# Performance work log

Hardware: AMD Instinct MI355X
Metric: run time of the kernel (lower is better)

## Reference

```python
import jax, jax.numpy as jnp
import numpy as np
from jax import lax

NUM_CLASSES = 80
STRIDES = (8, 16, 32, 64, 128)
PRE_NMS_THRESH = 0.05
PRE_NMS_TOPK = 1000
NMS_THRESH = 0.6
POST_NMS_TOPK = 100
NUM_CONVS = 4
CIN = 256
BATCH = 2
FEAT_SHAPES = ((100, 152), (50, 76), (25, 38), (13, 19), (7, 10))
CLASS_OFFSET = 10000.0  # coordinate offset for class-aware NMS


def conv3x3(x, w, b):
    # x: [B,C,H,W], w: [O,C,3,3] -> [B,O,H,W], stride 1, SAME padding
    y = lax.conv_general_dilated(x, w, (1, 1), 'SAME',
                                 dimension_numbers=('NCHW', 'OIHW', 'NCHW'))
    return y + b[None, :, None, None]


def tower(x, Ws, Bs):
    # sequence of (conv3x3 -> ReLU), norm='none'
    for i in range(Ws.shape[0]):
        x = jax.nn.relu(conv3x3(x, Ws[i], Bs[i]))
    return x


def compute_locations(h, w, stride):
    sx = jnp.arange(w, dtype=jnp.float32) * stride
    sy = jnp.arange(h, dtype=jnp.float32) * stride
    yy, xx = jnp.meshgrid(sy, sx, indexing='ij')
    return jnp.stack([xx.reshape(-1), yy.reshape(-1)], axis=1) + stride // 2  # [HW,2]


def nms_single(boxes, scores, classes):
    # boxes [N,4], scores [N] (>=0), classes [N] int. Greedy class-aware NMS.
    off = classes.astype(boxes.dtype) * CLASS_OFFSET
    b = boxes + off[:, None]
    area = (b[:, 2] - b[:, 0]) * (b[:, 3] - b[:, 1])

    def step(s, _):
        i = jnp.argmax(s)
        v = s[i]
        bi = b[i]
        lt = jnp.maximum(bi[:2], b[:, :2])
        rb = jnp.minimum(bi[2:], b[:, 2:])
        wh = jnp.maximum(rb - lt, 0.0)
        inter = wh[:, 0] * wh[:, 1]
        iou = inter / (area[i] + area - inter + 1e-9)
        s2 = jnp.where(iou > NMS_THRESH, -1.0, s).at[i].set(-1.0)
        return s2, (i, v)

    _, (idx, vals) = lax.scan(step, scores, None, length=POST_NMS_TOPK)
    valid = vals > 0.0
    out = jnp.concatenate(
        [boxes[idx], vals[:, None], classes[idx].astype(boxes.dtype)[:, None]], axis=1)
    return jnp.where(valid[:, None], out, 0.0)  # [POST_NMS_TOPK, 6]


def _forward(p3, p4, p5, p6, p7, cls_w, cls_b, box_w, box_b,
             logit_w, logit_b, pred_w, pred_b, ctr_w, ctr_b, scales):
    feats = (p3, p4, p5, p6, p7)
    boxes_all, scores_all, cls_all = [], [], []
    for l, x in enumerate(feats):
        # share_tower has 0 convs -> identity
        ct = tower(x, cls_w, cls_b)
        bt = tower(x, box_w, box_b)
        logits = conv3x3(ct, logit_w, logit_b)                   # [B,C,H,W]
        ctr = conv3x3(bt, ctr_w, ctr_b)                          # [B,1,H,W]
        reg = jax.nn.relu(conv3x3(bt, pred_w, pred_b) * scales[l])  # [B,4,H,W]
        B, _, H, W = logits.shape
        HW = H * W
        locs = compute_locations(H, W, STRIDES[l])               # [HW,2]
        cls_prob = jax.nn.sigmoid(logits).transpose(0, 2, 3, 1).reshape(B, HW, NUM_CLASSES)
        ctr_prob = jax.nn.sigmoid(ctr).reshape(B, HW, 1)
        s = cls_prob * ctr_prob                                  # thresh_with_ctr
        s = jnp.where(s > PRE_NMS_THRESH, s, 0.0)
        k = min(PRE_NMS_TOPK, HW * NUM_CLASSES)
        vals, idx = lax.top_k(s.reshape(B, HW * NUM_CLASSES), k)
        loc_idx = idx // NUM_CLASSES                             # [B,k]
        cls_idx = idx % NUM_CLASSES
        reg_f = reg.transpose(0, 2, 3, 1).reshape(B, HW, 4)
        reg_sel = jnp.take_along_axis(reg_f, loc_idx[..., None], axis=1)  # [B,k,4]
        loc_sel = locs[loc_idx]                                  # [B,k,2]
        boxes = jnp.stack([loc_sel[..., 0] - reg_sel[..., 0],
                           loc_sel[..., 1] - reg_sel[..., 1],
                           loc_sel[..., 0] + reg_sel[..., 2],
                           loc_sel[..., 1] + reg_sel[..., 3]], axis=-1)
        boxes_all.append(boxes)
        scores_all.append(jnp.sqrt(jnp.maximum(vals, 1e-12)))
        cls_all.append(cls_idx)
    boxes = jnp.concatenate(boxes_all, axis=1)    # [B,N,4]
    scores = jnp.concatenate(scores_all, axis=1)  # [B,N]
    classes = jnp.concatenate(cls_all, axis=1)    # [B,N]
    return jax.vmap(nms_single)(boxes, scores, classes)  # [B,POST_NMS_TOPK,6]


def setup_inputs() -> dict:
    key = jax.random.key(0)
    ks = jax.random.split(key, 12)
    std = 0.05  # larger than fcos init std=0.01 so decoded scores exceed the threshold
    inp = {}
    for i, (h, w) in enumerate(FEAT_SHAPES):
        inp[f'p{i + 3}'] = jax.random.normal(ks[i], (BATCH, CIN, h, w), dtype=jnp.float32)
    inp['cls_w'] = jax.random.normal(ks[5], (NUM_CONVS, CIN, CIN, 3, 3), dtype=jnp.float32) * std
    inp['cls_b'] = jnp.zeros((NUM_CONVS, CIN), dtype=jnp.float32)
    inp['box_w'] = jax.random.normal(ks[6], (NUM_CONVS, CIN, CIN, 3, 3), dtype=jnp.float32) * std
    inp['box_b'] = jnp.zeros((NUM_CONVS, CIN), dtype=jnp.float32)
    inp['logit_w'] = jax.random.normal(ks[7], (NUM_CLASSES, CIN, 3, 3), dtype=jnp.float32) * std
    inp['logit_b'] = jnp.zeros((NUM_CLASSES,), dtype=jnp.float32)
    inp['pred_w'] = jax.random.normal(ks[8], (4, CIN, 3, 3), dtype=jnp.float32) * std
    inp['pred_b'] = jnp.zeros((4,), dtype=jnp.float32)
    inp['ctr_w'] = jax.random.normal(ks[9], (1, CIN, 3, 3), dtype=jnp.float32) * std
    inp['ctr_b'] = jnp.zeros((1,), dtype=jnp.float32)
    inp['scales'] = jnp.ones((5,), dtype=jnp.float32)
    return inp


def reference(p3, p4, p5, p6, p7, cls_w, cls_b, box_w, box_b,
              logit_w, logit_b, pred_w, pred_b, ctr_w, ctr_b, scales):
    return _forward(p3, p4, p5, p6, p7, cls_w, cls_b, box_w, box_b,
                    logit_w, logit_b, pred_w, pred_b, ctr_w, ctr_b, scales)
```

## Files before the change

kernel.cpp:

```cpp
#include <hip/hip_runtime.h>
#include <stdint.h>
#include <math.h>

#define NCLS 80
#define TOTHW 20267

typedef _Float16 f16x8 __attribute__((ext_vector_type(8)));
typedef float f32x4 __attribute__((ext_vector_type(4)));
typedef short s16x8 __attribute__((ext_vector_type(8)));

static constexpr int cLW[5]    = {152,76,38,19,10};
static constexpr int cLH[5]    = {100,50,25,13,7};
static constexpr int cLHW[5]   = {15200,3800,950,247,70};
static constexpr int cLCUM[5]  = {0,15200,19000,19950,20197};
static constexpr int cLSTR[5]  = {8,16,32,64,128};
static constexpr int cCB[11]   = {0,123,246,278,310,319,328,331,334,335,336};
static constexpr int cPBASE[11]= {0,15744,31488,35584,39680,40832,41984,42368,42752,42880,43008};
static constexpr int cRCUM[11] = {0,100,200,250,300,325,350,363,376,383,390};
static constexpr int cCPX64[6] = {0,475,594,624,632,635};
#define NPXB64 635
#define SBE 11010048ull

__device__ __forceinline__ void split2(float y, unsigned short& h0, unsigned short& h1) {
  _Float16 b0 = (_Float16)y;
  float f0 = (float)b0;
  _Float16 b1 = (_Float16)((y - f0) * 2048.0f);
  h0 = __builtin_bit_cast(unsigned short, b0);
  h1 = __builtin_bit_cast(unsigned short, b1);
}

__device__ __forceinline__ void lds_hist_add(uint32_t* h, uint32_t bucket) {
  unsigned long long act = __ballot(1);
  int lane = (int)(threadIdx.x & 63u);
  int leader = __ffsll(act) - 1;
  uint32_t lb = (uint32_t)__shfl((int)bucket, leader, 64);
  unsigned long long same = __ballot(bucket == lb);
  if (same == act) {
    if (lane == leader) atomicAdd(&h[bucket], (uint32_t)__popcll(act));
  } else {
    atomicAdd(&h[bucket], 1u);
  }
}

__global__ void k_zero(unsigned short* X0, unsigned short* X1) {
  int px = blockIdx.x * 256 + threadIdx.x;
  if (px >= 43008) return;
  int pi = 0;
#pragma unroll
  for (int i = 1; i < 10; i++) if (px >= cPBASE[i]) pi = i;
  const int l = pi >> 1;
  const int p = px - cPBASE[pi];
  const int W = cLW[l], H = cLH[l], PWl = W + 2;
  const int pr = p / PWl, pc = p - pr * PWl;
  if (pr >= 1 && pr <= H && pc >= 1 && pc <= W) return;
  s16x8 z = {0,0,0,0,0,0,0,0};
  size_t base = (size_t)px * 256;
#pragma unroll
  for (int k = 0; k < 32; k++) {
    *reinterpret_cast<s16x8*>(X0 + base + k*8) = z;
    *reinterpret_cast<s16x8*>(X1 + base + k*8) = z;
  }
}

__global__ __launch_bounds__(256)
void k_prep(const float* __restrict__ p0, const float* __restrict__ p1,
            const float* __restrict__ p2, const float* __restrict__ p3,
            const float* __restrict__ p4,
            unsigned short* __restrict__ X0, unsigned short* __restrict__ X1) {
  int bx = blockIdx.x;
  int pi = 0;
#pragma unroll
  for (int i = 1; i < 10; i++) if (bx >= cRCUM[i]) pi = i;
  const int h = bx - cRCUM[pi];
  const int l = pi >> 1, bidx = pi & 1;
  const int W = cLW[l], HW = cLHW[l], PWl = W + 2;
  const int PB = cPBASE[pi];
  const float* src;
  if (l == 0) src = p0; else if (l == 1) src = p1; else if (l == 2) src = p2;
  else if (l == 3) src = p3; else src = p4;
  src += (size_t)bidx * 256 * HW;
  const int tid = threadIdx.x;
  __shared__ float tile[64][152];
  for (int c0 = 0; c0 < 256; c0 += 64) {
    {
      int c = tid >> 2, wq = tid & 3;
      for (int w = wq; w < W; w += 4)
        tile[c][w] = src[(size_t)(c0 + c) * HW + h * W + w];
    }
    __syncthreads();
    {
      int c8 = (tid & 7) * 8;
      for (int w = tid >> 3; w < W; w += 32) {
        size_t base = (size_t)(PB + (h + 1) * PWl + (w + 1)) * 256 + c0 + c8;
        unsigned short a0[8], a1[8];
#pragma unroll
        for (int j = 0; j < 8; j++) split2(tile[c8 + j][w], a0[j], a1[j]);
        *reinterpret_cast<s16x8*>(X0 + base) = *reinterpret_cast<s16x8*>(a0);
        *reinterpret_cast<s16x8*>(X1 + base) = *reinterpret_cast<s16x8*>(a1);
      }
    }
    __syncthreads();
  }
}

__global__ void k_pack(const float* __restrict__ w, unsigned short* __restrict__ wp) {
  const int oc = blockIdx.x, c = threadIdx.x;
#pragma unroll
  for (int r = 0; r < 9; r++) {
    float v = w[((size_t)oc * 256 + c) * 9 + r];
    unsigned short h0, h1;
    split2(v, h0, h1);
    wp[((size_t)(r * 2 + 0) * 256 + oc) * 256 + c] = h0;
    wp[((size_t)(r * 2 + 1) * 256 + oc) * 256 + c] = h1;
  }
}

__global__ void k_packhead(const float* __restrict__ ctw, const float* __restrict__ pdw,
                           float* __restrict__ wh) {
  const int r = blockIdx.x, c = threadIdx.x;
  float* d = &wh[((size_t)r * 256 + c) * 5];
  d[0] = ctw[c * 9 + r];
#pragma unroll
  for (int q = 0; q < 4; q++) d[1 + q] = pdw[(size_t)q * 2304 + c * 9 + r];
}

struct MfArgs {
  const unsigned short *X0, *X1;
  const unsigned short *Wp;
  const float* bias;
  unsigned short *Y0, *Y1;
  float* actf;
  float* scores;
  const float* ctrp;
  uint32_t* hist;
};

template<int EPI>
__global__ __launch_bounds__(256, 2)
void conv_mfma(MfArgs a) {
  __shared__ __align__(16) unsigned short lds[18432];
  const int tid = threadIdx.x;
  const int lane = tid & 63;
  const int wid = tid >> 6;

  const int nwg = (EPI == 2) ? 336 : 672;
  const int id = blockIdx.x;
  const int w = (id & 7) * (nwg >> 3) + (id >> 3);
  const int oc0 = (EPI == 2) ? 0 : (w & 1) * 128;
  int bx = (EPI == 2) ? w : (w >> 1);

  int pi = 0;
#pragma unroll
  for (int i = 1; i < 10; i++) if (bx >= cCB[i]) pi = i;
  const int l = pi >> 1, bidx = pi & 1;
  const int pxb = bx - cCB[pi];
  const int px0 = pxb * 128;
  const int PB = cPBASE[pi];
  const int W = cLW[l], H = cLH[l], HW = cLHW[l], PWl = W + 2;

  int row_[2], g_[2];
#pragma unroll
  for (int d = 0; d < 2; d++) {
    int idx2 = tid + d * 256;
    row_[d] = idx2 >> 2;
    g_[d] = idx2 & 3;
  }

  const int wr = wid >> 1, wc = wid & 1;
  const int kg = lane >> 4, ln15 = lane & 15;
  int fA[4], fB[4];
#pragma unroll
  for (int mt = 0; mt < 4; mt++) fA[mt] = (wr * 64 + mt * 16 + ln15) * 72 + kg * 8;
#pragma unroll
  for (int nt = 0; nt < 4; nt++) fB[nt] = 9216 + (wc * 64 + nt * 16 + ln15) * 72 + kg * 8;

  f32x4 acc0[4][4], acc1[4][4];
#pragma unroll
  for (int mt = 0; mt < 4; mt++)
#pragma unroll
    for (int nt = 0; nt < 4; nt++) {
      acc0[mt][nt] = (f32x4){0.f, 0.f, 0.f, 0.f};
      acc1[mt][nt] = (f32x4){0.f, 0.f, 0.f, 0.f};
    }

  s16x8 ra[4], rb[4];
  auto loadstep = [&](int step) {
    const int rr = step >> 3;
    const int c0 = (step & 7) << 5;
    const int dh = rr / 3 - 1, dw = rr - (rr / 3) * 3 - 1;
    const long long OFF = (long long)(PB + px0 + dh * PWl + dw);
#pragma unroll
    for (int s = 0; s < 2; s++) {
      const unsigned short* Xs = (s == 0) ? a.X0 : a.X1;
      const unsigned short* Ws = a.Wp + (size_t)(rr * 2 + s) * 65536;
#pragma unroll
      for (int d = 0; d < 2; d++) {
        ra[s * 2 + d] = *reinterpret_cast<const s16x8*>(Xs + (OFF + row_[d]) * 256 + c0 + g_[d] * 8);
        rb[s * 2 + d] = *reinterpret_cast<const s16x8*>(Ws + (size_t)(oc0 + row_[d]) * 256 + c0 + g_[d] * 8);
      }
    }
  };

  loadstep(0);
  for (int step = 0; step < 72; ++step) {
    if (step) __syncthreads();
#pragma unroll
    for (int s = 0; s < 2; s++)
#pragma unroll
      for (int d = 0; d < 2; d++) {
        const int o = row_[d] * 72 + (s * 4 + g_[d]) * 8;
        *reinterpret_cast<s16x8*>(&lds[o]) = ra[s * 2 + d];
        *reinterpret_cast<s16x8*>(&lds[o + 9216]) = rb[s * 2 + d];
      }
    __syncthreads();
    if (step != 71) loadstep(step + 1);

    f16x8 bv[4][2];
#pragma unroll
    for (int nt = 0; nt < 4; nt++) {
      bv[nt][0] = *reinterpret_cast<const f16x8*>(&lds[fB[nt]]);
      bv[nt][1] = *reinterpret_cast<const f16x8*>(&lds[fB[nt] + 32]);
    }
#pragma unroll
    for (int mt = 0; mt < 4; mt++) {
      f16x8 av0 = *reinterpret_cast<const f16x8*>(&lds[fA[mt]]);
      f16x8 av1 = *reinterpret_cast<const f16x8*>(&lds[fA[mt] + 32]);
#pragma unroll
      for (int nt = 0; nt < 4; nt++) {
        acc0[mt][nt] = __builtin_amdgcn_mfma_f32_16x16x32_f16(av0, bv[nt][0], acc0[mt][nt], 0, 0, 0);
        acc1[mt][nt] = __builtin_amdgcn_mfma_f32_16x16x32_f16(av0, bv[nt][1], acc1[mt][nt], 0, 0, 0);
        acc1[mt][nt] = __builtin_amdgcn_mfma_f32_16x16x32_f16(av1, bv[nt][0], acc1[mt][nt], 0, 0, 0);
      }
    }
  }
  __syncthreads();

  uint32_t* hh = nullptr;
  if (EPI == 2) {
    hh = reinterpret_cast<uint32_t*>(lds);
    for (int i = tid; i < 4096; i += 256) hh[i] = 0;
    __syncthreads();
  }
#pragma unroll
  for (int mt = 0; mt < 4; mt++) {
#pragma unroll
    for (int i = 0; i < 4; i++) {
      const int pxl = wr * 64 + mt * 16 + (lane >> 4) * 4 + i;
      const int p = px0 + pxl;
      const int pr = p / PWl, pc = p - pr * PWl;
      if (!(pr >= 1 && pr <= H && pc >= 1 && pc <= W)) continue;
      const int hw = (pr - 1) * W + (pc - 1);
#pragma unroll
      for (int nt = 0; nt < 4; nt++) {
        const int oc = oc0 + wc * 64 + nt * 16 + ln15;
        const float v = acc0[mt][nt][i] + acc1[mt][nt][i] * 4.8828125e-4f;
        if (EPI == 2) {
          if (oc < NCLS) {
            float y = v + a.bias[oc];
            float pcs = 1.0f / (1.0f + expf(-y));
            float s = pcs * a.ctrp[2 * cLCUM[l] + bidx * HW + hw];
            s = (s > 0.05f) ? s : 0.f;
            a.scores[(size_t)NCLS * (2 * cLCUM[l] + bidx * HW) + (size_t)oc * HW + hw] = s;
            lds_hist_add(hh, __float_as_uint(s) >> 20);
          }
        } else {
          float y = fmaxf(v + a.bias[oc], 0.f);
          if (EPI == 0) {
            size_t o = (size_t)(PB + p) * 256 + oc;
            unsigned short h0, h1;
            split2(y, h0, h1);
            a.Y0[o] = h0; a.Y1[o] = h1;
          } else {
            a.actf[(size_t)(PB + p) * 256 + oc] = y;
          }
        }
      }
    }
  }
  if (EPI == 2) {
    __syncthreads();
    uint32_t* gh = a.hist + (size_t)(l * 2 + bidx) * 4096;
    for (int i = tid; i < 4096; i += 256) { uint32_t v = hh[i]; if (v) atomicAdd(&gh[i], v); }
  }
}

__global__ __launch_bounds__(256)
void k_head2(const float* __restrict__ headact, const float* __restrict__ wh,
             const float* __restrict__ ctb, const float* __restrict__ pdb,
             const float* __restrict__ scl,
             float* __restrict__ ctrp, float* __restrict__ regb) {
  __shared__ float swh[11520];
  for (int i = threadIdx.x; i < 11520; i += 256) swh[i] = wh[i];
  int bx = blockIdx.x; int l = 0;
#pragma unroll
  for (int i = 1; i < 5; i++) if (bx >= cCPX64[i]) l = i;
  const int lblk = bx - cCPX64[l];
  const int H = cLH[l], W = cLW[l], HW = cLHW[l]; const int N = 2 * HW;
  const int lane = threadIdx.x & 63;
  const int wv = threadIdx.x >> 6;
  __syncthreads();
  const float bb0 = ctb[0], bb1 = pdb[0], bb2 = pdb[1], bb3 = pdb[2], bb4 = pdb[3];
  const float sc = scl[l];
  const int c4 = lane * 4;
  for (int t = 0; t < 16; ++t) {
    int px = lblk * 64 + wv * 16 + t;
    if (px >= N) break;
    int bb = px / HW; int hw = px - bb * HW; int hh = hw / W; int ww = hw - hh * W;
    const int PB = cPBASE[l * 2 + bb];
    float a0 = 0.f, a1 = 0.f, a2 = 0.f, a3 = 0.f, a4 = 0.f;
#pragma unroll
    for (int r = 0; r < 9; r++) {
      int dh = r / 3 - 1, dw = r % 3 - 1;
      int ih = hh + dh, iw = ww + dw;
      if (!(((unsigned)ih < (unsigned)H) && ((unsigned)iw < (unsigned)W))) continue;
      const float4 x = *reinterpret_cast<const float4*>(
          headact + (size_t)(PB + (ih + 1) * (W + 2) + (iw + 1)) * 256 + c4);
      const float* wr = &swh[(size_t)(r * 256 + c4) * 5];
      a0 = fmaf(x.x, wr[0],  a0); a1 = fmaf(x.x, wr[1],  a1); a2 = fmaf(x.x, wr[2],  a2);
      a3 = fmaf(x.x, wr[3],  a3); a4 = fmaf(x.x, wr[4],  a4);
      a0 = fmaf(x.y, wr[5],  a0); a1 = fmaf(x.y, wr[6],  a1); a2 = fmaf(x.y, wr[7],  a2);
      a3 = fmaf(x.y, wr[8],  a3); a4 = fmaf(x.y, wr[9],  a4);
      a0 = fmaf(x.z, wr[10], a0); a1 = fmaf(x.z, wr[11], a1); a2 = fmaf(x.z, wr[12], a2);
      a3 = fmaf(x.z, wr[13], a3); a4 = fmaf(x.z, wr[14], a4);
      a0 = fmaf(x.w, wr[15], a0); a1 = fmaf(x.w, wr[16], a1); a2 = fmaf(x.w, wr[17], a2);
      a3 = fmaf(x.w, wr[18], a3); a4 = fmaf(x.w, wr[19], a4);
    }
#pragma unroll
    for (int off = 32; off > 0; off >>= 1) {
      a0 += __shfl_xor(a0, off, 64); a1 += __shfl_xor(a1, off, 64); a2 += __shfl_xor(a2, off, 64);
      a3 += __shfl_xor(a3, off, 64); a4 += __shfl_xor(a4, off, 64);
    }
    if (lane == 0) {
      const int gi = 2 * cLCUM[l] + bb * HW + hw;
      ctrp[gi] = 1.0f / (1.0f + expf(-(a0 + bb0)));
      float* rg = regb + (size_t)gi * 4;
      rg[0] = fmaxf((a1 + bb1) * sc, 0.f);
      rg[1] = fmaxf((a2 + bb2) * sc, 0.f);
      rg[2] = fmaxf((a3 + bb3) * sc, 0.f);
      rg[3] = fmaxf((a4 + bb4) * sc, 0.f);
    }
  }
}

__global__ void k_init(uint32_t* __restrict__ hist, uint32_t* __restrict__ ctrA,
                       uint32_t* __restrict__ ctrB) {
  int i = blockIdx.x * blockDim.x + threadIdx.x;
  if (i < 40960) hist[i] = 0;
  if (i < 10) { ctrA[i] = 0; ctrB[i] = 0; }
}

__global__ __launch_bounds__(256)
void k_select(const uint32_t* __restrict__ hist, int* __restrict__ meta) {
  const int sid = blockIdx.x;
  const uint32_t* gh = hist + (size_t)sid * 4096;
  __shared__ uint32_t ps[256];
  uint32_t sum = 0;
  for (int i = 0; i < 16; i++) sum += gh[threadIdx.x * 16 + i];
  ps[threadIdx.x] = sum;
  __syncthreads();
  if (threadIdx.x == 0) {
    uint32_t c = 0; int T = 0, m = 1000;
    for (int ch = 255; ch >= 0; --ch) {
      if (c + ps[ch] >= 1000u) {
        for (int t = ch * 16 + 15; t >= ch * 16; --t) {
          uint32_t hv = gh[t];
          if (c + hv >= 1000u) { T = t; m = (int)(1000u - c); break; }
          c += hv;
        }
        break;
      }
      c += ps[ch];
    }
    meta[sid * 4 + 0] = T;
    meta[sid * 4 + 1] = (int)c;
    meta[sid * 4 + 2] = m;
    meta[sid * 4 + 3] = (int)gh[T];
  }
}

__global__ __launch_bounds__(256)
void k_collect(const float* __restrict__ scores, const int* __restrict__ meta,
               unsigned long long* __restrict__ listA, unsigned long long* __restrict__ listB,
               uint32_t* __restrict__ ctrA, uint32_t* __restrict__ ctrB) {
  const int sid = blockIdx.y; const int l = sid >> 1, b = sid & 1;
  const int HW = cLHW[l]; const int size = NCLS * HW;
  const int base = blockIdx.x * 4096;
  if (base >= size) return;
  const size_t sbase = (size_t)NCLS * (2 * cLCUM[l] + b * HW);
  const float* sb = scores + sbase;
  unsigned long long* lB = listB + sbase;
  unsigned long long* lA = listA + (size_t)sid * 1024;
  const uint32_t T = (uint32_t)meta[sid * 4];
  const int lane = (int)(threadIdx.x & 63u);
  __shared__ uint32_t cA, cB, bA, bB;
  if (threadIdx.x == 0) { cA = 0; cB = 0; }
  __syncthreads();
  uint32_t wa = 0, wb = 0;
  for (int j = 0; j < 16; j++) {
    int i = base + threadIdx.x + j * 256;
    bool inb = (i < size);
    uint32_t bits = inb ? __float_as_uint(sb[i]) : 0u;
    uint32_t bkt = bits >> 20;
    unsigned long long mA = __ballot(inb && bkt > T);
    unsigned long long mB = __ballot(inb && bkt == T);
    if (lane == 0) { wa += (uint32_t)__popcll(mA); wb += (uint32_t)__popcll(mB); }
  }
  if (lane == 0) { if (wa) atomicAdd(&cA, wa); if (wb) atomicAdd(&cB, wb); }
  __syncthreads();
  if (threadIdx.x == 0) {
    bA = cA ? atomicAdd(&ctrA[sid], cA) : 0u;
    bB = cB ? atomicAdd(&ctrB[sid], cB) : 0u;
    cA = 0; cB = 0;
  }
  __syncthreads();
  for (int j = 0; j < 16; j++) {
    int i = base + threadIdx.x + j * 256;
    bool inb = (i < size);
    uint32_t bits = inb ? __float_as_uint(sb[i]) : 0u;
    uint32_t bkt = bits >> 20;
    bool pA = inb && bkt > T;
    bool pB = inb && bkt == T;
    unsigned long long key = 0;
    if (pA || pB) {
      int cls = i / HW; int hw = i - cls * HW;
      uint32_t idx = (uint32_t)(hw * NCLS + cls);
      key = ((unsigned long long)bits << 32) | (unsigned long long)(0xFFFFFFFFu - idx);
    }
    unsigned long long mA = __ballot(pA);
    unsigned long long mB = __ballot(pB);
    unsigned long long lt = (1ull << lane) - 1ull;
    if (mA) {
// ... 32 lines not shown
  unsigned long long prefix = 0, mask = 0;
  for (int p = 7; p >= 0; --p) {
    for (int i = threadIdx.x; i < 256; i += 1024) h[i] = 0;
    __syncthreads();
    for (int i = threadIdx.x; i < nB; i += 1024) {
      unsigned long long k = lB[i];
      if ((k & mask) == prefix) {
        uint32_t bkt = (uint32_t)((k >> (p * 8)) & 255ull);
        lds_hist_add(h, bkt);
      }
    }
    __syncthreads();
    if (threadIdx.x == 0) {
      uint32_t c = 0; int sel = 0; int mnew = m;
      for (int t = 255; t >= 0; --t) {
        if (c + h[t] >= (uint32_t)m) { sel = t; mnew = m - (int)c; break; }
        c += h[t];
      }
      sPre = prefix | ((unsigned long long)sel << (p * 8));
      sM = mnew;
    }
    __syncthreads();
    prefix = sPre; m = sM;
    mask |= (0xFFull << (p * 8));
    __syncthreads();
  }
  if (threadIdx.x == 0) sCnt = ctrA[sid];
  __syncthreads();
  for (int i = threadIdx.x; i < nB; i += 1024) {
    unsigned long long k = lB[i];
    if (k >= prefix) {
      uint32_t pos = atomicAdd(&sCnt, 1u);
      if (pos < 1024u) listA[(size_t)sid * 1024 + pos] = k;
    }
  }
  __syncthreads();
  if (threadIdx.x == 0) ctrA[sid] = sCnt;
}

__global__ __launch_bounds__(256)
void k_sortdec(const unsigned long long* __restrict__ listA, const uint32_t* __restrict__ ctrA,
               const float* __restrict__ regb, float* __restrict__ cbox,
               float* __restrict__ cscr, float* __restrict__ ccls) {
  const int sid = blockIdx.x; const int l = sid >> 1, b = sid & 1;
  const int HW = cLHW[l], W = cLW[l];
  __shared__ unsigned long long key[1024];
  int n = (int)ctrA[sid]; if (n > 1024) n = 1024;
  for (int i = threadIdx.x; i < 1024; i += 256)
    key[i] = (i < n) ? listA[(size_t)sid * 1024 + i] : 0ull;
  __syncthreads();
  for (int len = 2; len <= 1024; len <<= 1) {
    for (int j = len >> 1; j > 0; j >>= 1) {
      for (int t = threadIdx.x; t < 512; t += 256) {
        int i = ((t & ~(j - 1)) << 1) | (t & (j - 1));
        int pp = i | j;
        unsigned long long a = key[i], bq = key[pp];
        bool desc = ((i & len) == 0);
        if ((a < bq) == desc) { key[i] = bq; key[pp] = a; }
      }
      __syncthreads();
    }
  }
  for (int r = threadIdx.x; r < 1000; r += 256) {
    unsigned long long k = key[r];
    uint32_t bits = (uint32_t)(k >> 32);
    uint32_t idx = 0xFFFFFFFFu - (uint32_t)(k & 0xFFFFFFFFull);
    float val = __uint_as_float(bits);
    float sc = sqrtf(fmaxf(val, 1e-12f));
    int cls = (int)(idx % NCLS); int loc = (int)(idx / NCLS);
    int hh = loc / W; int ww = loc - hh * W;
    float cx = (float)(ww * cLSTR[l] + (cLSTR[l] >> 1));
    float cy = (float)(hh * cLSTR[l] + (cLSTR[l] >> 1));
    const float* rg = regb + (size_t)(2 * cLCUM[l] + b * HW + loc) * 4;
    int slot = b * 5000 + l * 1000 + r;
    cbox[slot * 4 + 0] = cx - rg[0];
    cbox[slot * 4 + 1] = cy - rg[1];
    cbox[slot * 4 + 2] = cx + rg[2];
    cbox[slot * 4 + 3] = cy + rg[3];
    cscr[slot] = sc;
    ccls[slot] = (float)cls;
  }
}

__global__ __launch_bounds__(1024)
void k_nms(const float* __restrict__ cbox, const float* __restrict__ cscr,
           const float* __restrict__ ccls, float* __restrict__ out) {
  const int b = blockIdx.x;
  const int tid = threadIdx.x;
  __shared__ float s[5000];
  __shared__ float wv[16]; __shared__ int wi[16];
  __shared__ float bbx[5]; __shared__ int sBi; __shared__ float sBv;
  float x1[5], y1[5], x2[5], y2[5], ar[5];
#pragma unroll
  for (int r = 0; r < 5; r++) {
    int j = tid + r * 1024;
    if (j < 5000) {
      const float4 bx = *reinterpret_cast<const float4*>(cbox + ((size_t)b * 5000 + j) * 4);
      float off = ccls[b * 5000 + j] * 10000.0f;
      x1[r] = bx.x + off; y1[r] = bx.y + off; x2[r] = bx.z + off; y2[r] = bx.w + off;
      ar[r] = (x2[r] - x1[r]) * (y2[r] - y1[r]);
      s[j] = cscr[b * 5000 + j];
    }
  }
  __syncthreads();
  for (int it = 0; it < 100; ++it) {
    float best = -1e30f; int bi = 0x7FFFFFFF;
#pragma unroll
    for (int r = 0; r < 5; r++) {
      int j = tid + r * 1024;
      if (j < 5000) {
        float v = s[j];
        if (v > best || (v == best && j < bi)) { best = v; bi = j; }
      }
    }
    for (int o = 32; o > 0; o >>= 1) {
      float ov = __shfl_down(best, o, 64); int oi = __shfl_down(bi, o, 64);
      if (ov > best || (ov == best && oi < bi)) { best = ov; bi = oi; }
    }
    if ((tid & 63) == 0) { wv[tid >> 6] = best; wi[tid >> 6] = bi; }
    __syncthreads();
    if (tid < 64) {
      float v = (tid < 16) ? wv[tid] : -1e30f; int ix = (tid < 16) ? wi[tid] : 0x7FFFFFFF;
      for (int o = 8; o > 0; o >>= 1) {
        float ov = __shfl_down(v, o, 64); int oi = __shfl_down(ix, o, 64);
        if (ov > v || (ov == v && oi < ix)) { v = ov; ix = oi; }
      }
      if (tid == 0) { sBi = ix; sBv = v; }
    }
    __syncthreads();
    const int pick = sBi; const float pv = sBv;
    if (tid == (pick & 1023)) {
      const int r = pick >> 10;
      bbx[0] = x1[r]; bbx[1] = y1[r]; bbx[2] = x2[r]; bbx[3] = y2[r]; bbx[4] = ar[r];
      float* orow = out + ((size_t)b * 100 + it) * 6;
      if (pv > 0.f) {
        const float4 obx = *reinterpret_cast<const float4*>(cbox + ((size_t)b * 5000 + pick) * 4);
        orow[0] = obx.x; orow[1] = obx.y; orow[2] = obx.z; orow[3] = obx.w;
        orow[4] = pv; orow[5] = ccls[b * 5000 + pick];
      } else {
        orow[0] = 0.f; orow[1] = 0.f; orow[2] = 0.f; orow[3] = 0.f; orow[4] = 0.f; orow[5] = 0.f;
      }
    }
    __syncthreads();
    const float bx1 = bbx[0], by1 = bbx[1], bx2 = bbx[2], by2 = bbx[3], ba = bbx[4];
#pragma unroll
    for (int r = 0; r < 5; r++) {
      int j = tid + r * 1024;
      if (j < 5000) {
        float ix1 = fmaxf(bx1, x1[r]), iy1 = fmaxf(by1, y1[r]);
        float ix2 = fminf(bx2, x2[r]), iy2 = fminf(by2, y2[r]);
        float iw = fmaxf(ix2 - ix1, 0.f), ih = fmaxf(iy2 - iy1, 0.f);
        float inter = iw * ih;
        float iou = inter / ((ba + ar[r] - inter) + 1e-9f);
        if (iou > 0.6f || j == pick) s[j] = -1.0f;
      }
    }
    __syncthreads();
  }
}

static inline size_t alignup(size_t x) { return (x + 255) & ~(size_t)255; }

extern "C" void kernel_launch(void* const* d_in, const int* in_sizes, int n_in,
                              void* d_out, int out_size, void* d_ws, size_t ws_size,
                              hipStream_t stream) {
  (void)in_sizes; (void)n_in; (void)out_size; (void)ws_size;
  const float* p0 = (const float*)d_in[0];
  const float* p1 = (const float*)d_in[1];
  const float* p2 = (const float*)d_in[2];
  const float* p3 = (const float*)d_in[3];
  const float* p4 = (const float*)d_in[4];
  const float* cls_w   = (const float*)d_in[5];
  const float* cls_b   = (const float*)d_in[6];
  const float* box_w   = (const float*)d_in[7];
  const float* box_b   = (const float*)d_in[8];
  const float* logit_w = (const float*)d_in[9];
  const float* logit_b = (const float*)d_in[10];
  const float* pred_w  = (const float*)d_in[11];
  const float* pred_b  = (const float*)d_in[12];
  const float* ctr_w   = (const float*)d_in[13];
  const float* ctr_b   = (const float*)d_in[14];
  const float* scales  = (const float*)d_in[15];

  char* base = (char*)d_ws;
  size_t off = 0;
  auto take = [&](size_t bytes) { void* p = base + off; off = alignup(off + bytes); return p; };
  float* regb = (float*)take((size_t)4 * 2 * TOTHW * 4);
  float* ctrp = (float*)take((size_t)2 * TOTHW * 4);
  uint32_t* hist = (uint32_t*)take((size_t)40960 * 4);
  int* meta = (int*)take((size_t)40 * 4);
  uint32_t* ctrA = (uint32_t*)take(256);
  uint32_t* ctrB = (uint32_t*)take(256);
  unsigned long long* listA = (unsigned long long*)take((size_t)10 * 1024 * 8);
  float* cbox = (float*)take((size_t)2 * 5000 * 16);
  float* cscr = (float*)take((size_t)2 * 5000 * 4);
  float* ccls = (float*)take((size_t)2 * 5000 * 4);
  float* wh   = (float*)take((size_t)9 * 256 * 5 * 4);
  unsigned short* wpack = (unsigned short*)take((size_t)9 * 2 * 256 * 256 * 2);
  unsigned short* R1_0 = (unsigned short*)take(SBE * 2);
  unsigned short* R1_1 = (unsigned short*)take(SBE * 2);
  unsigned short* R2_0 = (unsigned short*)take(SBE * 2);
  unsigned short* R2_1 = (unsigned short*)take(SBE * 2);
  (void)take(65536);
  float* scores = (float*)R2_0;
  unsigned long long* listB = (unsigned long long*)R1_0;
  float* headact = (float*)R1_0;

  const size_t WSTRIDE = (size_t)256 * 2304;

  hipLaunchKernelGGL(k_init, dim3(160), dim3(256), 0, stream, hist, ctrA, ctrB);
  hipLaunchKernelGGL(k_packhead, dim3(9), dim3(256), 0, stream, ctr_w, pred_w, wh);
  hipLaunchKernelGGL(k_zero, dim3(168), dim3(256), 0, stream, R1_0, R1_1);
  hipLaunchKernelGGL(k_zero, dim3(168), dim3(256), 0, stream, R2_0, R2_1);
  hipLaunchKernelGGL(k_prep, dim3(390), dim3(256), 0, stream, p0, p1, p2, p3, p4, R1_0, R1_1);

  auto runConv = [&](int epi, const unsigned short* x0, const unsigned short* x1,
                     const float* bias, unsigned short* y0, unsigned short* y1,
                     float* af, float* sc) {
    MfArgs a;
    a.X0 = x0; a.X1 = x1; a.Wp = wpack; a.bias = bias;
    a.Y0 = y0; a.Y1 = y1; a.actf = af; a.scores = sc; a.ctrp = ctrp;
    a.hist = hist;
    if (epi == 0)      hipLaunchKernelGGL(conv_mfma<0>, dim3(672), dim3(256), 0, stream, a);
    else if (epi == 1) hipLaunchKernelGGL(conv_mfma<1>, dim3(672), dim3(256), 0, stream, a);
    else               hipLaunchKernelGGL(conv_mfma<2>, dim3(336), dim3(256), 0, stream, a);
  };

  hipLaunchKernelGGL(k_pack, dim3(256), dim3(256), 0, stream, box_w + 0 * WSTRIDE, wpack);
  runConv(0, R1_0, R1_1, box_b + 0,   R2_0, R2_1, nullptr, nullptr);
  hipLaunchKernelGGL(k_pack, dim3(256), dim3(256), 0, stream, box_w + 1 * WSTRIDE, wpack);
  runConv(0, R2_0, R2_1, box_b + 256, R1_0, R1_1, nullptr, nullptr);
  hipLaunchKernelGGL(k_pack, dim3(256), dim3(256), 0, stream, box_w + 2 * WSTRIDE, wpack);
  runConv(0, R1_0, R1_1, box_b + 512, R2_0, R2_1, nullptr, nullptr);
  hipLaunchKernelGGL(k_pack, dim3(256), dim3(256), 0, stream, box_w + 3 * WSTRIDE, wpack);
  runConv(1, R2_0, R2_1, box_b + 768, nullptr, nullptr, headact, nullptr);
  hipLaunchKernelGGL(k_head2, dim3(NPXB64), dim3(256), 0, stream, headact, wh, ctr_b,
                     pred_b, scales, ctrp, regb);

  hipLaunchKernelGGL(k_zero, dim3(168), dim3(256), 0, stream, R1_0, R1_1);
  hipLaunchKernelGGL(k_prep, dim3(390), dim3(256), 0, stream, p0, p1, p2, p3, p4, R1_0, R1_1);
  hipLaunchKernelGGL(k_pack, dim3(256), dim3(256), 0, stream, cls_w + 0 * WSTRIDE, wpack);
  runConv(0, R1_0, R1_1, cls_b + 0,   R2_0, R2_1, nullptr, nullptr);
  hipLaunchKernelGGL(k_pack, dim3(256), dim3(256), 0, stream, cls_w + 1 * WSTRIDE, wpack);
  runConv(0, R2_0, R2_1, cls_b + 256, R1_0, R1_1, nullptr, nullptr);
  hipLaunchKernelGGL(k_pack, dim3(256), dim3(256), 0, stream, cls_w + 2 * WSTRIDE, wpack);
  runConv(0, R1_0, R1_1, cls_b + 512, R2_0, R2_1, nullptr, nullptr);
  hipLaunchKernelGGL(k_pack, dim3(256), dim3(256), 0, stream, cls_w + 3 * WSTRIDE, wpack);
  runConv(0, R2_0, R2_1, cls_b + 768, R1_0, R1_1, nullptr, nullptr);
  hipLaunchKernelGGL(k_pack, dim3(80), dim3(256), 0, stream, logit_w, wpack);
  runConv(2, R1_0, R1_1, logit_b, nullptr, nullptr, nullptr, scores);

  hipLaunchKernelGGL(k_select,  dim3(10), dim3(256), 0, stream, hist, meta);
  hipLaunchKernelGGL(k_collect, dim3(297, 10), dim3(256), 0, stream, scores, meta, listA, listB, ctrA, ctrB);
  hipLaunchKernelGGL(k_refine,  dim3(10), dim3(1024), 0, stream, meta, listB, listA, ctrA);
  hipLaunchKernelGGL(k_sortdec, dim3(10), dim3(256), 0, stream, listA, ctrA, regb, cbox, cscr, ccls);
  hipLaunchKernelGGL(k_nms,     dim3(2), dim3(1024), 0, stream, cbox, cscr, ccls, (float*)d_out);
}
```

Baseline: 2.245 ms.

## Channel-block activation layout, direct-to-register MFMA loads, prepacked weights, per-class parallel NMS

Activations move to a channel-chunked layout (8 chunks of 32 channels) and weights are pre-swizzled into MFMA fragment order, so the conv kernel loads operands straight from global memory into registers. This drops the LDS staging and the per-step barriers. All nine weight layers are packed once in a single launch instead of before each conv. The serial 100-iteration greedy NMS is replaced by a per-class parallel NMS followed by a radix top-100 selection, which is exact because offset boxes of different classes never overlap. The risk is that losing LDS reuse raises global and L2 traffic, since each wave now refetches its A and B fragments.

```diff
diff --git a/kernel.cpp b/kernel.cpp
--- a/kernel.cpp
+++ b/kernel.cpp
@@ -4,6 +4,8 @@
 
 #define NCLS 80
 #define TOTHW 20267
+#define CHS 1376256
+#define WLAYER 1179648ull
 
 typedef _Float16 f16x8 __attribute__((ext_vector_type(8)));
 typedef float f32x4 __attribute__((ext_vector_type(4)));
@@ -54,11 +56,14 @@
   const int pr = p / PWl, pc = p - pr * PWl;
   if (pr >= 1 && pr <= H && pc >= 1 && pc <= W) return;
   s16x8 z = {0,0,0,0,0,0,0,0};
-  size_t base = (size_t)px * 256;
-#pragma unroll
-  for (int k = 0; k < 32; k++) {
-    *reinterpret_cast<s16x8*>(X0 + base + k*8) = z;
-    *reinterpret_cast<s16x8*>(X1 + base + k*8) = z;
+#pragma unroll
+  for (int ch = 0; ch < 8; ch++) {
+    size_t base = (size_t)ch * CHS + (size_t)px * 32;
+#pragma unroll
+    for (int q = 0; q < 4; q++) {
+      *reinterpret_cast<s16x8*>(X0 + base + q*8) = z;
+      *reinterpret_cast<s16x8*>(X1 + base + q*8) = z;
+    }
   }
 }
 
@@ -90,8 +95,10 @@
     __syncthreads();
     {
       int c8 = (tid & 7) * 8;
+      const int c = c0 + c8;
+      const size_t cb = (size_t)(c >> 5) * CHS + (c & 31);
       for (int w = tid >> 3; w < W; w += 32) {
-        size_t base = (size_t)(PB + (h + 1) * PWl + (w + 1)) * 256 + c0 + c8;
+        size_t base = cb + (size_t)(PB + (h + 1) * PWl + (w + 1)) * 32;
         unsigned short a0[8], a1[8];
 #pragma unroll
         for (int j = 0; j < 8; j++) split2(tile[c8 + j][w], a0[j], a1[j]);
@@ -103,15 +110,27 @@
   }
 }
 
-__global__ void k_pack(const float* __restrict__ w, unsigned short* __restrict__ wp) {
+__global__ void k_packall(const float* __restrict__ box_w, const float* __restrict__ cls_w,
+                          const float* __restrict__ logit_w, unsigned short* __restrict__ wp) {
+  const int layer = blockIdx.y;
   const int oc = blockIdx.x, c = threadIdx.x;
+  const float* w; int Cout = 256;
+  const size_t WSTRIDE = (size_t)256 * 2304;
+  if (layer < 4)      w = box_w + (size_t)layer * WSTRIDE;
+  else if (layer < 8) w = cls_w + (size_t)(layer - 4) * WSTRIDE;
+  else { w = logit_w; Cout = NCLS; }
+  if (oc >= Cout) return;
+  unsigned short* wpL = wp + (size_t)layer * WLAYER;
+  const int ocf = oc >> 4, ln = oc & 15;
+  const int kc = c >> 5, kg = (c >> 3) & 3, e = c & 7;
+  const int lane = kg * 16 + ln;
 #pragma unroll
   for (int r = 0; r < 9; r++) {
     float v = w[((size_t)oc * 256 + c) * 9 + r];
     unsigned short h0, h1;
     split2(v, h0, h1);
-    wp[((size_t)(r * 2 + 0) * 256 + oc) * 256 + c] = h0;
-    wp[((size_t)(r * 2 + 1) * 256 + oc) * 256 + c] = h1;
+    wpL[((((size_t)(r * 2 + 0) * 16 + ocf) * 8 + kc) * 64 + lane) * 8 + e] = h0;
+    wpL[((((size_t)(r * 2 + 1) * 16 + ocf) * 8 + kc) * 64 + lane) * 8 + e] = h1;
   }
 }
 
@@ -138,7 +157,7 @@
 template<int EPI>
 __global__ __launch_bounds__(256, 2)
 void conv_mfma(MfArgs a) {
-  __shared__ __align__(16) unsigned short lds[18432];
+  __shared__ uint32_t hh[4096];
   const int tid = threadIdx.x;
   const int lane = tid & 63;
   const int wid = tid >> 6;
@@ -158,21 +177,10 @@
   const int PB = cPBASE[pi];
   const int W = cLW[l], H = cLH[l], HW = cLHW[l], PWl = W + 2;
 
-  int row_[2], g_[2];
-#pragma unroll
-  for (int d = 0; d < 2; d++) {
-    int idx2 = tid + d * 256;
-    row_[d] = idx2 >> 2;
-    g_[d] = idx2 & 3;
-  }
-
   const int wr = wid >> 1, wc = wid & 1;
   const int kg = lane >> 4, ln15 = lane & 15;
-  int fA[4], fB[4];
-#pragma unroll
-  for (int mt = 0; mt < 4; mt++) fA[mt] = (wr * 64 + mt * 16 + ln15) * 72 + kg * 8;
-#pragma unroll
-  for (int nt = 0; nt < 4; nt++) fB[nt] = 9216 + (wc * 64 + nt * 16 + ln15) * 72 + kg * 8;
+  const int ocfb = (oc0 >> 4) + wc * 4;
+  const long rowbase = (long)(px0 + wr * 64 + ln15) + PB;
 
   f32x4 acc0[4][4], acc1[4][4];
 #pragma unroll
@@ -183,61 +191,34 @@
       acc1[mt][nt] = (f32x4){0.f, 0.f, 0.f, 0.f};
     }
 
-  s16x8 ra[4], rb[4];
-  auto loadstep = [&](int step) {
-    const int rr = step >> 3;
-    const int c0 = (step & 7) << 5;
-    const int dh = rr / 3 - 1, dw = rr - (rr / 3) * 3 - 1;
-    const long long OFF = (long long)(PB + px0 + dh * PWl + dw);
-#pragma unroll
-    for (int s = 0; s < 2; s++) {
-      const unsigned short* Xs = (s == 0) ? a.X0 : a.X1;
-      const unsigned short* Ws = a.Wp + (size_t)(rr * 2 + s) * 65536;
-#pragma unroll
-      for (int d = 0; d < 2; d++) {
-        ra[s * 2 + d] = *reinterpret_cast<const s16x8*>(Xs + (OFF + row_[d]) * 256 + c0 + g_[d] * 8);
-        rb[s * 2 + d] = *reinterpret_cast<const s16x8*>(Ws + (size_t)(oc0 + row_[d]) * 256 + c0 + g_[d] * 8);
-      }
-    }
-  };
-
-  loadstep(0);
   for (int step = 0; step < 72; ++step) {
-    if (step) __syncthreads();
-#pragma unroll
-    for (int s = 0; s < 2; s++)
-#pragma unroll
-      for (int d = 0; d < 2; d++) {
-        const int o = row_[d] * 72 + (s * 4 + g_[d]) * 8;
-        *reinterpret_cast<s16x8*>(&lds[o]) = ra[s * 2 + d];
-        *reinterpret_cast<s16x8*>(&lds[o + 9216]) = rb[s * 2 + d];
-      }
-    __syncthreads();
-    if (step != 71) loadstep(step + 1);
-
-    f16x8 bv[4][2];
+    const int rr = step >> 3, cc = step & 7;
+    const int r3 = rr / 3;
+    const long shift = (long)(r3 - 1) * PWl + (rr - r3 * 3 - 1);
+    f16x8 av[4][2], bv[4][2];
+#pragma unroll
+    for (int mt = 0; mt < 4; mt++) {
+      const long ao = (long)cc * CHS + (rowbase + shift + mt * 16) * 32 + kg * 8;
+      av[mt][0] = *reinterpret_cast<const f16x8*>(a.X0 + ao);
+      av[mt][1] = *reinterpret_cast<const f16x8*>(a.X1 + ao);
+    }
 #pragma unroll
     for (int nt = 0; nt < 4; nt++) {
-      bv[nt][0] = *reinterpret_cast<const f16x8*>(&lds[fB[nt]]);
-      bv[nt][1] = *reinterpret_cast<const f16x8*>(&lds[fB[nt] + 32]);
-    }
-#pragma unroll
-    for (int mt = 0; mt < 4; mt++) {
-      f16x8 av0 = *reinterpret_cast<const f16x8*>(&lds[fA[mt]]);
-      f16x8 av1 = *reinterpret_cast<const f16x8*>(&lds[fA[mt] + 32]);
+      const size_t bo = ((size_t)((rr * 2) * 16 + ocfb + nt) * 8 + cc) * 512 + lane * 8;
+      bv[nt][0] = *reinterpret_cast<const f16x8*>(a.Wp + bo);
+      bv[nt][1] = *reinterpret_cast<const f16x8*>(a.Wp + bo + 65536);
+    }
+#pragma unroll
+    for (int mt = 0; mt < 4; mt++)
 #pragma unroll
       for (int nt = 0; nt < 4; nt++) {
-        acc0[mt][nt] = __builtin_amdgcn_mfma_f32_16x16x32_f16(av0, bv[nt][0], acc0[mt][nt], 0, 0, 0);
-        acc1[mt][nt] = __builtin_amdgcn_mfma_f32_16x16x32_f16(av0, bv[nt][1], acc1[mt][nt], 0, 0, 0);
-        acc1[mt][nt] = __builtin_amdgcn_mfma_f32_16x16x32_f16(av1, bv[nt][0], acc1[mt][nt], 0, 0, 0);
-      }
-    }
-  }
-  __syncthreads();
-
-  uint32_t* hh = nullptr;
+        acc0[mt][nt] = __builtin_amdgcn_mfma_f32_16x16x32_f16(av[mt][0], bv[nt][0], acc0[mt][nt], 0, 0, 0);
+        acc1[mt][nt] = __builtin_amdgcn_mfma_f32_16x16x32_f16(av[mt][0], bv[nt][1], acc1[mt][nt], 0, 0, 0);
+        acc1[mt][nt] = __builtin_amdgcn_mfma_f32_16x16x32_f16(av[mt][1], bv[nt][0], acc1[mt][nt], 0, 0, 0);
+      }
+  }
+
   if (EPI == 2) {
-    hh = reinterpret_cast<uint32_t*>(lds);
     for (int i = tid; i < 4096; i += 256) hh[i] = 0;
     __syncthreads();
   }
@@ -266,7 +247,7 @@
         } else {
           float y = fmaxf(v + a.bias[oc], 0.f);
           if (EPI == 0) {
-            size_t o = (size_t)(PB + p) * 256 + oc;
+            size_t o = (size_t)(oc >> 5) * CHS + (size_t)(PB + p) * 32 + (oc & 31);
             unsigned short h0, h1;
             split2(y, h0, h1);
             a.Y0[o] = h0; a.Y1[o] = h1;
@@ -343,10 +324,11 @@
 }
 
 __global__ void k_init(uint32_t* __restrict__ hist, uint32_t* __restrict__ ctrA,
-                       uint32_t* __restrict__ ctrB) {
+                       uint32_t* __restrict__ ctrB, uint32_t* __restrict__ survCnt) {
   int i = blockIdx.x * blockDim.x + threadIdx.x;
   if (i < 40960) hist[i] = 0;
   if (i < 10) { ctrA[i] = 0; ctrB[i] = 0; }
+  if (i < 2) survCnt[i] = 0;
 }
 
 __global__ __launch_bounds__(256)
@@ -545,80 +527,167 @@
   }
 }
 
+__global__ __launch_bounds__(256)
+void k_nmscls(const float* __restrict__ cbox, const float* __restrict__ cscr,
+              const float* __restrict__ ccls,
+              unsigned long long* __restrict__ surv, uint32_t* __restrict__ survCnt) {
+  const int cls = blockIdx.x;
+  const int b = blockIdx.y;
+  __shared__ unsigned short mslot[5024];
+  __shared__ float ms[5024];
+  __shared__ uint32_t mcnt;
+  __shared__ int sPick; __shared__ float sPickV;
+  __shared__ float pb[5];
+  __shared__ float wvv[4]; __shared__ int wvi[4];
+  if (threadIdx.x == 0) mcnt = 0;
+  __syncthreads();
+  const float fc = (float)cls;
+  for (int j = threadIdx.x; j < 5000; j += 256) {
+    if (ccls[b * 5000 + j] == fc) {
+      uint32_t p = atomicAdd(&mcnt, 1u);
+      mslot[p] = (unsigned short)j;
+      ms[p] = cscr[b * 5000 + j];
+    }
+  }
+  __syncthreads();
+  const int n = (int)mcnt;
+  if (n == 0) return;
+  const float off = fc * 10000.0f;
+  const int lane = threadIdx.x & 63, wv = threadIdx.x >> 6;
+  for (;;) {
+    float best = -1.f; int bi = 0x7FFF; int bidx = 0;
+    for (int i = threadIdx.x; i < n; i += 256) {
+      float v = ms[i];
+      int sl = mslot[i];
+      if (v > best || (v == best && sl < bi)) { best = v; bi = sl; bidx = i; }
+    }
+    for (int o = 32; o > 0; o >>= 1) {
+      float ov = __shfl_down(best, o, 64);
+      int oi = __shfl_down(bi, o, 64);
+      int ox = __shfl_down(bidx, o, 64);
+      if (ov > best || (ov == best && oi < bi)) { best = ov; bi = oi; bidx = ox; }
+    }
+    if (lane == 0) { wvv[wv] = best; wvi[wv] = (bidx << 13) | bi; }
+    __syncthreads();
+    if (threadIdx.x == 0) {
+      float bb = wvv[0]; int pk = wvi[0];
+      for (int q = 1; q < 4; q++) {
+        float v = wvv[q]; int c = wvi[q];
+        if (v > bb || (v == bb && (c & 8191) < (pk & 8191))) { bb = v; pk = c; }
+      }
+      sPickV = bb; sPick = pk;
+      if (bb >= 0.f) {
+        int slot = pk & 8191;
+        uint32_t bits = __float_as_uint(bb);
+        uint32_t gslot = (uint32_t)(b * 5000 + slot);
+        unsigned long long key = ((unsigned long long)bits << 32) |
+                                 (unsigned long long)(0xFFFFFFFFu - gslot);
+        uint32_t pos = atomicAdd(&survCnt[b], 1u);
+        surv[(size_t)b * 5000 + pos] = key;
+        const float4 bx = *reinterpret_cast<const float4*>(cbox + (size_t)gslot * 4);
+        pb[0] = bx.x + off; pb[1] = bx.y + off; pb[2] = bx.z + off; pb[3] = bx.w + off;
+        pb[4] = (pb[2] - pb[0]) * (pb[3] - pb[1]);
+      }
+    }
+    __syncthreads();
+    if (sPickV < 0.f) break;
+    const int pidx = sPick >> 13;
+    const float bx1 = pb[0], by1 = pb[1], bx2 = pb[2], by2 = pb[3], ba = pb[4];
+    for (int i = threadIdx.x; i < n; i += 256) {
+      float v = ms[i];
+      if (v < 0.f) continue;
+      int sl = mslot[i];
+      const float4 bq = *reinterpret_cast<const float4*>(cbox + ((size_t)b * 5000 + sl) * 4);
+      float x1 = bq.x + off, y1 = bq.y + off, x2 = bq.z + off, y2 = bq.w + off;
+      float ar = (x2 - x1) * (y2 - y1);
+      float ix1 = fmaxf(bx1, x1), iy1 = fmaxf(by1, y1);
+      float ix2 = fminf(bx2, x2), iy2 = fminf(by2, y2);
+      float iw = fmaxf(ix2 - ix1, 0.f), ih = fmaxf(iy2 - iy1, 0.f);
+      float inter = iw * ih;
+      float iou = inter / ((ba + ar - inter) + 1e-9f);
+      if (iou > 0.6f || i == pidx) ms[i] = -1.0f;
+    }
+    __syncthreads();
+  }
+}
+
 __global__ __launch_bounds__(1024)
-void k_nms(const float* __restrict__ cbox, const float* __restrict__ cscr,
-           const float* __restrict__ ccls, float* __restrict__ out) {
+void k_nmsfinal(const unsigned long long* __restrict__ surv, const uint32_t* __restrict__ survCnt,
+                const float* __restrict__ cbox, const float* __restrict__ ccls,
+                float* __restrict__ out) {
   const int b = blockIdx.x;
-  const int tid = threadIdx.x;
-  __shared__ float s[5000];
-  __shared__ float wv[16]; __shared__ int wi[16];
-  __shared__ float bbx[5]; __shared__ int sBi; __shared__ float sBv;
-  float x1[5], y1[5], x2[5], y2[5], ar[5];
-#pragma unroll
-  for (int r = 0; r < 5; r++) {
-    int j = tid + r * 1024;
-    if (j < 5000) {
-      const float4 bx = *reinterpret_cast<const float4*>(cbox + ((size_t)b * 5000 + j) * 4);
-      float off = ccls[b * 5000 + j] * 10000.0f;
-      x1[r] = bx.x + off; y1[r] = bx.y + off; x2[r] = bx.z + off; y2[r] = bx.w + off;
-      ar[r] = (x2[r] - x1[r]) * (y2[r] - y1[r]);
-      s[j] = cscr[b * 5000 + j];
-    }
-  }
-  __syncthreads();
-  for (int it = 0; it < 100; ++it) {
-    float best = -1e30f; int bi = 0x7FFFFFFF;
-#pragma unroll
-    for (int r = 0; r < 5; r++) {
-      int j = tid + r * 1024;
-      if (j < 5000) {
-        float v = s[j];
-        if (v > best || (v == best && j < bi)) { best = v; bi = j; }
-      }
-    }
-    for (int o = 32; o > 0; o >>= 1) {
-      float ov = __shfl_down(best, o, 64); int oi = __shfl_down(bi, o, 64);
-      if (ov > best || (ov == best && oi < bi)) { best = ov; bi = oi; }
-    }
-    if ((tid & 63) == 0) { wv[tid >> 6] = best; wi[tid >> 6] = bi; }
-    __syncthreads();
-    if (tid < 64) {
-      float v = (tid < 16) ? wv[tid] : -1e30f; int ix = (tid < 16) ? wi[tid] : 0x7FFFFFFF;
-      for (int o = 8; o > 0; o >>= 1) {
-        float ov = __shfl_down(v, o, 64); int oi = __shfl_down(ix, o, 64);
-        if (ov > v || (ov == v && oi < ix)) { v = ov; ix = oi; }
-      }
-      if (tid == 0) { sBi = ix; sBv = v; }
-    }
-    __syncthreads();
-    const int pick = sBi; const float pv = sBv;
-    if (tid == (pick & 1023)) {
-      const int r = pick >> 10;
-      bbx[0] = x1[r]; bbx[1] = y1[r]; bbx[2] = x2[r]; bbx[3] = y2[r]; bbx[4] = ar[r];
-      float* orow = out + ((size_t)b * 100 + it) * 6;
-      if (pv > 0.f) {
-        const float4 obx = *reinterpret_cast<const float4*>(cbox + ((size_t)b * 5000 + pick) * 4);
-        orow[0] = obx.x; orow[1] = obx.y; orow[2] = obx.z; orow[3] = obx.w;
-        orow[4] = pv; orow[5] = ccls[b * 5000 + pick];
-      } else {
-        orow[0] = 0.f; orow[1] = 0.f; orow[2] = 0.f; orow[3] = 0.f; orow[4] = 0.f; orow[5] = 0.f;
-      }
-    }
-    __syncthreads();
-    const float bx1 = bbx[0], by1 = bbx[1], bx2 = bbx[2], by2 = bbx[3], ba = bbx[4];
-#pragma unroll
-    for (int r = 0; r < 5; r++) {
-      int j = tid + r * 1024;
-      if (j < 5000) {
-        float ix1 = fmaxf(bx1, x1[r]), iy1 = fmaxf(by1, y1[r]);
-        float ix2 = fminf(bx2, x2[r]), iy2 = fminf(by2, y2[r]);
-        float iw = fmaxf(ix2 - ix1, 0.f), ih = fmaxf(iy2 - iy1, 0.f);
-        float inter = iw * ih;
-        float iou = inter / ((ba + ar[r] - inter) + 1e-9f);
-        if (iou > 0.6f || j == pick) s[j] = -1.0f;
-      }
-    }
-    __syncthreads();
+  const int n = (int)survCnt[b];
+  const unsigned long long* sv = surv + (size_t)b * 5000;
+  const int m = n < 100 ? n : 100;
+  __shared__ uint32_t h[256];
+  __shared__ unsigned long long sPre; __shared__ int sM;
+  __shared__ unsigned long long topk[128];
+  __shared__ uint32_t tcnt;
+  unsigned long long prefix = 0, mask = 0;
+  int mm = m;
+  if (m > 0) {
+    for (int p = 7; p >= 0; --p) {
+      for (int i = threadIdx.x; i < 256; i += 1024) h[i] = 0;
+      __syncthreads();
+      for (int i = threadIdx.x; i < n; i += 1024) {
+        unsigned long long k = sv[i];
+        if ((k & mask) == prefix) lds_hist_add(h, (uint32_t)((k >> (p * 8)) & 255ull));
+      }
+      __syncthreads();
+      if (threadIdx.x == 0) {
+        uint32_t c = 0; int sel = 0; int mnew = mm;
+        for (int t = 255; t >= 0; --t) {
+          if (c + h[t] >= (uint32_t)mm) { sel = t; mnew = mm - (int)c; break; }
+          c += h[t];
+        }
+        sPre = prefix | ((unsigned long long)sel << (p * 8));
+        sM = mnew;
+      }
+      __syncthreads();
+      prefix = sPre; mm = sM;
+      mask |= (0xFFull << (p * 8));
+      __syncthreads();
+    }
+  }
+  if (threadIdx.x == 0) tcnt = 0;
+  for (int i = threadIdx.x; i < 128; i += 1024) topk[i] = 0;
+  __syncthreads();
+  if (m > 0) {
+    for (int i = threadIdx.x; i < n; i += 1024) {
+      unsigned long long k = sv[i];
+      if (k >= prefix) {
+        uint32_t p = atomicAdd(&tcnt, 1u);
+        if (p < 128) topk[p] = k;
+      }
+    }
+  }
+  __syncthreads();
+  for (int len = 2; len <= 128; len <<= 1) {
+    for (int j = len >> 1; j > 0; j >>= 1) {
+      for (int t = threadIdx.x; t < 64; t += 1024) {
+        int i = ((t & ~(j - 1)) << 1) | (t & (j - 1));
+        int pp = i | j;
+        unsigned long long a = topk[i], bq = topk[pp];
+        bool desc = ((i & len) == 0);
+        if ((a < bq) == desc) { topk[i] = bq; topk[pp] = a; }
+      }
+      __syncthreads();
+    }
+  }
+  if (threadIdx.x < 100) {
+    int it = threadIdx.x;
+    float* orow = out + ((size_t)b * 100 + it) * 6;
+    if (it < m) {
+      unsigned long long k = topk[it];
+      uint32_t gslot = 0xFFFFFFFFu - (uint32_t)(k & 0xFFFFFFFFull);
+      const float4 bx = *reinterpret_cast<const float4*>(cbox + (size_t)gslot * 4);
+      orow[0] = bx.x; orow[1] = bx.y; orow[2] = bx.z; orow[3] = bx.w;
+      orow[4] = __uint_as_float((uint32_t)(k >> 32));
+      orow[5] = ccls[gslot];
+    } else {
+      orow[0] = 0.f; orow[1] = 0.f; orow[2] = 0.f;
+      orow[3] = 0.f; orow[4] = 0.f; orow[5] = 0.f;
+    }
   }
 }
 
@@ -654,12 +723,14 @@
   int* meta = (int*)take((size_t)40 * 4);
   uint32_t* ctrA = (uint32_t*)take(256);
   uint32_t* ctrB = (uint32_t*)take(256);
+  uint32_t* survCnt = (uint32_t*)take(256);
   unsigned long long* listA = (unsigned long long*)take((size_t)10 * 1024 * 8);
+  unsigned long long* surv = (unsigned long long*)take((size_t)2 * 5000 * 8);
   float* cbox = (float*)take((size_t)2 * 5000 * 16);
   float* cscr = (float*)take((size_t)2 * 5000 * 4);
   float* ccls = (float*)take((size_t)2 * 5000 * 4);
   float* wh   = (float*)take((size_t)9 * 256 * 5 * 4);
-  unsigned short* wpack = (unsigned short*)take((size_t)9 * 2 * 256 * 256 * 2);
+  unsigned short* wpackF = (unsigned short*)take((size_t)9 * WLAYER * 2);
   unsigned short* R1_0 = (unsigned short*)take(SBE * 2);
   unsigned short* R1_1 = (unsigned short*)take(SBE * 2);
   unsigned short* R2_0 = (unsigned short*)take(SBE * 2);
@@ -669,19 +740,18 @@
   unsigned long long* listB = (unsigned long long*)R1_0;
   float* headact = (float*)R1_0;
 
-  const size_t WSTRIDE = (size_t)256 * 2304;
-
-  hipLaunchKernelGGL(k_init, dim3(160), dim3(256), 0, stream, hist, ctrA, ctrB);
+  hipLaunchKernelGGL(k_init, dim3(160), dim3(256), 0, stream, hist, ctrA, ctrB, survCnt);
   hipLaunchKernelGGL(k_packhead, dim3(9), dim3(256), 0, stream, ctr_w, pred_w, wh);
+  hipLaunchKernelGGL(k_packall, dim3(256, 9), dim3(256), 0, stream, box_w, cls_w, logit_w, wpackF);
   hipLaunchKernelGGL(k_zero, dim3(168), dim3(256), 0, stream, R1_0, R1_1);
   hipLaunchKernelGGL(k_zero, dim3(168), dim3(256), 0, stream, R2_0, R2_1);
   hipLaunchKernelGGL(k_prep, dim3(390), dim3(256), 0, stream, p0, p1, p2, p3, p4, R1_0, R1_1);
 
-  auto runConv = [&](int epi, const unsigned short* x0, const unsigned short* x1,
+  auto runConv = [&](int epi, int layer, const unsigned short* x0, const unsigned short* x1,
                      const float* bias, unsigned short* y0, unsigned short* y1,
                      float* af, float* sc) {
     MfArgs a;
-    a.X0 = x0; a.X1 = x1; a.Wp = wpack; a.bias = bias;
+    a.X0 = x0; a.X1 = x1; a.Wp = wpackF + (size_t)layer * WLAYER; a.bias = bias;
     a.Y0 = y0; a.Y1 = y1; a.actf = af; a.scores = sc; a.ctrp = ctrp;
     a.hist = hist;
     if (epi == 0)      hipLaunchKernelGGL(conv_mfma<0>, dim3(672), dim3(256), 0, stream, a);
@@ -689,33 +759,25 @@
     else               hipLaunchKernelGGL(conv_mfma<2>, dim3(336), dim3(256), 0, stream, a);
   };
 
-  hipLaunchKernelGGL(k_pack, dim3(256), dim3(256), 0, stream, box_w + 0 * WSTRIDE, wpack);
-  runConv(0, R1_0, R1_1, box_b + 0,   R2_0, R2_1, nullptr, nullptr);
-  hipLaunchKernelGGL(k_pack, dim3(256), dim3(256), 0, stream, box_w + 1 * WSTRIDE, wpack);
-  runConv(0, R2_0, R2_1, box_b + 256, R1_0, R1_1, nullptr, nullptr);
-  hipLaunchKernelGGL(k_pack, dim3(256), dim3(256), 0, stream, box_w + 2 * WSTRIDE, wpack);
-  runConv(0, R1_0, R1_1, box_b + 512, R2_0, R2_1, nullptr, nullptr);
-  hipLaunchKernelGGL(k_pack, dim3(256), dim3(256), 0, stream, box_w + 3 * WSTRIDE, wpack);
-  runConv(1, R2_0, R2_1, box_b + 768, nullptr, nullptr, headact, nullptr);
+  runConv(0, 0, R1_0, R1_1, box_b + 0,   R2_0, R2_1, nullptr, nullptr);
+  runConv(0, 1, R2_0, R2_1, box_b + 256, R1_0, R1_1, nullptr, nullptr);
+  runConv(0, 2, R1_0, R1_1, box_b + 512, R2_0, R2_1, nullptr, nullptr);
+  runConv(1, 3, R2_0, R2_1, box_b + 768, nullptr, nullptr, headact, nullptr);
   hipLaunchKernelGGL(k_head2, dim3(NPXB64), dim3(256), 0, stream, headact, wh, ctr_b,
                      pred_b, scales, ctrp, regb);
 
   hipLaunchKernelGGL(k_zero, dim3(168), dim3(256), 0, stream, R1_0, R1_1);
   hipLaunchKernelGGL(k_prep, dim3(390), dim3(256), 0, stream, p0, p1, p2, p3, p4, R1_0, R1_1);
-  hipLaunchKernelGGL(k_pack, dim3(256), dim3(256), 0, stream, cls_w + 0 * WSTRIDE, wpack);
-  runConv(0, R1_0, R1_1, cls_b + 0,   R2_0, R2_1, nullptr, nullptr);
-  hipLaunchKernelGGL(k_pack, dim3(256), dim3(256), 0, stream, cls_w + 1 * WSTRIDE, wpack);
-  runConv(0, R2_0, R2_1, cls_b + 256, R1_0, R1_1, nullptr, nullptr);
-  hipLaunchKernelGGL(k_pack, dim3(256), dim3(256), 0, stream, cls_w + 2 * WSTRIDE, wpack);
-  runConv(0, R1_0, R1_1, cls_b + 512, R2_0, R2_1, nullptr, nullptr);
-  hipLaunchKernelGGL(k_pack, dim3(256), dim3(256), 0, stream, cls_w + 3 * WSTRIDE, wpack);
-  runConv(0, R2_0, R2_1, cls_b + 768, R1_0, R1_1, nullptr, nullptr);
-  hipLaunchKernelGGL(k_pack, dim3(80), dim3(256), 0, stream, logit_w, wpack);
-  runConv(2, R1_0, R1_1, logit_b, nullptr, nullptr, nullptr, scores);
+  runConv(0, 4, R1_0, R1_1, cls_b + 0,   R2_0, R2_1, nullptr, nullptr);
+  runConv(0, 5, R2_0, R2_1, cls_b + 256, R1_0, R1_1, nullptr, nullptr);
+  runConv(0, 6, R1_0, R1_1, cls_b + 512, R2_0, R2_1, nullptr, nullptr);
+  runConv(0, 7, R2_0, R2_1, cls_b + 768, R1_0, R1_1, nullptr, nullptr);
+  runConv(2, 8, R1_0, R1_1, logit_b, nullptr, nullptr, nullptr, scores);
 
   hipLaunchKernelGGL(k_select,  dim3(10), dim3(256), 0, stream, hist, meta);
   hipLaunchKernelGGL(k_collect, dim3(297, 10), dim3(256), 0, stream, scores, meta, listA, listB, ctrA, ctrB);
   hipLaunchKernelGGL(k_refine,  dim3(10), dim3(1024), 0, stream, meta, listB, listA, ctrA);
   hipLaunchKernelGGL(k_sortdec, dim3(10), dim3(256), 0, stream, listA, ctrA, regb, cbox, cscr, ccls);
-  hipLaunchKernelGGL(k_nms,     dim3(2), dim3(1024), 0, stream, cbox, cscr, ccls, (float*)d_out);
-}
+  hipLaunchKernelGGL(k_nmscls,  dim3(NCLS, 2), dim3(256), 0, stream, cbox, cscr, ccls, surv, survCnt);
+  hipLaunchKernelGGL(k_nmsfinal, dim3(2), dim3(1024), 0, stream, surv, survCnt, cbox, ccls, (float*)d_out);
+}
```

After: 2.703 ms. +20.4%, slower.
